# Kernel optimization log

Measured on AMD Instinct MI355X. Metric: run time of the kernel, lower is better.

## Reference

```python
import jax, jax.numpy as jnp
import numpy as np

EPS = 1e-5
PDIM, QKD, DIM = 64, 16, 256
SCALE = QKD ** -0.5


def setup_inputs() -> dict:
    key = jax.random.key(0)
    ks = jax.random.split(key, 13)
    B, H, W = 8, 64, 64
    return {
        "x": jax.random.normal(ks[0], (B, DIM, H, W), jnp.float32),
        "gn_g": jax.random.uniform(ks[1], (PDIM,), jnp.float32, 0.5, 1.5),
        "gn_b": jax.random.normal(ks[2], (PDIM,), jnp.float32) * 0.1,
        "qkv_w": jax.random.normal(ks[3], (2 * QKD + PDIM, PDIM), jnp.float32) * (PDIM ** -0.5),
        "qkv_bn_g": jax.random.uniform(ks[4], (2 * QKD + PDIM,), jnp.float32, 0.5, 1.5),
        "qkv_bn_b": jax.random.normal(ks[5], (2 * QKD + PDIM,), jnp.float32) * 0.1,
        "qkv_rm": jax.random.normal(ks[6], (2 * QKD + PDIM,), jnp.float32) * 0.1,
        "qkv_rv": jax.random.uniform(ks[7], (2 * QKD + PDIM,), jnp.float32, 0.5, 1.5),
        "proj_w": jax.random.normal(ks[8], (DIM, DIM), jnp.float32) * (DIM ** -0.5),
        "proj_bn_g": jax.random.uniform(ks[9], (DIM,), jnp.float32, 0.5, 1.5),
        "proj_bn_b": jax.random.normal(ks[10], (DIM,), jnp.float32) * 0.1,
        "proj_rm": jax.random.normal(ks[11], (DIM,), jnp.float32) * 0.1,
        "proj_rv": jax.random.uniform(ks[12], (DIM,), jnp.float32, 0.5, 1.5),
    }


def _bn(y, g, b, rm, rv):
    # inference BatchNorm over channel axis 1 of [B,C,H,W]
    inv = g / jnp.sqrt(rv + EPS)
    return y * inv[None, :, None, None] + (b - rm * inv)[None, :, None, None]


def reference(x, gn_g, gn_b, qkv_w, qkv_bn_g, qkv_bn_b, qkv_rm, qkv_rv,
              proj_w, proj_bn_g, proj_bn_b, proj_rm, proj_rv):
    B, C, H, W = x.shape
    x1, x2 = x[:, :PDIM], x[:, PDIM:]
    # GroupNorm with 1 group: normalize over (C,H,W) per sample
    mu = jnp.mean(x1, axis=(1, 2, 3), keepdims=True)
    var = jnp.var(x1, axis=(1, 2, 3), keepdims=True)
    x1n = (x1 - mu) / jnp.sqrt(var + EPS)
    x1n = x1n * gn_g[None, :, None, None] + gn_b[None, :, None, None]
    # qkv: 1x1 conv + BN
    qkv = jnp.einsum('bchw,oc->bohw', x1n, qkv_w)
    qkv = _bn(qkv, qkv_bn_g, qkv_bn_b, qkv_rm, qkv_rv)
    q, k, v = qkv[:, :QKD], qkv[:, QKD:2 * QKD], qkv[:, 2 * QKD:]
    N = H * W
    q = q.reshape(B, QKD, N)
    k = k.reshape(B, QKD, N)
    v = v.reshape(B, PDIM, N)
    attn = jnp.einsum('bcn,bcm->bnm', q, k) * SCALE  # [B,N,N]
    attn = jax.nn.softmax(attn, axis=-1)
    x1_attn = jnp.einsum('bcm,bnm->bcn', v, attn).reshape(B, PDIM, H, W)
    xc = jnp.concatenate([x1_attn, x2], axis=1)
    # proj: ReLU -> 1x1 conv -> BN
    y = jnp.einsum('bchw,oc->bohw', jax.nn.relu(xc), proj_w)
    return _bn(y, proj_bn_g, proj_bn_b, proj_rm, proj_rv)
```

## Files before the change

### kernel.cpp

```cpp
#include <hip/hip_runtime.h>
#include <hip/hip_bf16.h>

typedef __bf16 bf16;
typedef __bf16 bf16x4 __attribute__((ext_vector_type(4)));
typedef __bf16 bf16x8 __attribute__((ext_vector_type(8)));
typedef float  f32x16 __attribute__((ext_vector_type(16)));

#define MFMA32 __builtin_amdgcn_mfma_f32_32x32x16_bf16
#define EPSV 1e-5f
#define QSCALE 0.36067376022224085f

__device__ __forceinline__ f32x16 fzero16() {
  f32x16 z;
#pragma unroll
  for (int i = 0; i < 16; ++i) z[i] = 0.f;
  return z;
}

__device__ __forceinline__ void dma16(const void* g, void* s) {
  __builtin_amdgcn_global_load_lds(
      (const __attribute__((address_space(1))) void*)g,
      (__attribute__((address_space(3))) void*)s, 16, 0, 0);
}

__global__ __launch_bounds__(256) void k_stats_partial(const float* __restrict__ x,
                                                       float* __restrict__ part) {
  const int b = blockIdx.x >> 5, k = blockIdx.x & 31;
  const float* p = x + (size_t)b * 256 * 4096 + k * 8192;
  const int t = threadIdx.x;
  float s = 0.f, q = 0.f;
#pragma unroll
  for (int j = 0; j < 8; ++j) {
    float4 v = ((const float4*)p)[t + j * 256];
    s += v.x + v.y + v.z + v.w;
    q += v.x * v.x + v.y * v.y + v.z * v.z + v.w * v.w;
  }
  __shared__ float ls[256], lq[256];
  ls[t] = s; lq[t] = q;
  __syncthreads();
  for (int off = 128; off > 0; off >>= 1) {
    if (t < off) { ls[t] += ls[t + off]; lq[t] += lq[t + off]; }
    __syncthreads();
  }
  if (t == 0) { part[blockIdx.x * 2] = ls[0]; part[blockIdx.x * 2 + 1] = lq[0]; }
}

__global__ __launch_bounds__(256) void k_stats_final(const float* __restrict__ part,
                                                     float* __restrict__ stats) {
  const int t = threadIdx.x, b = t >> 5, k = t & 31;
  float s = part[(b * 32 + k) * 2], q = part[(b * 32 + k) * 2 + 1];
  for (int off = 16; off > 0; off >>= 1) {
    s += __shfl_down(s, off, 32);
    q += __shfl_down(q, off, 32);
  }
  if (k == 0) {
    const float inv_n = 1.f / 262144.f;
    const float mu = s * inv_n;
    const float var = q * inv_n - mu * mu;
    stats[b * 2] = mu;
    stats[b * 2 + 1] = rsqrtf(var + EPSV);
  }
}

__global__ __launch_bounds__(256) void k_qkv(
    const float* __restrict__ x, const float* __restrict__ gn_g, const float* __restrict__ gn_b,
    const float* __restrict__ qkv_w, const float* __restrict__ bn_g, const float* __restrict__ bn_b,
    const float* __restrict__ bn_rm, const float* __restrict__ bn_rv,
    const float* __restrict__ stats,
    bf16* __restrict__ qw, bf16* __restrict__ kw, bf16* __restrict__ vw) {
  const int b = blockIdx.x >> 6, tile = blockIdx.x & 63;
  const int n0 = tile * 64, t = threadIdx.x;
  __shared__ float xn[64][68];
  __shared__ float W[64][96];
  __shared__ float beta_s[96];
  const float mu = stats[b * 2], rstd = stats[b * 2 + 1];
  {
    const int c = t >> 2, f = t & 3;
    const float A = rstd * gn_g[c], B = gn_b[c] - mu * A;
    const float* xr = x + ((size_t)b * 256 + c) * 4096 + n0;
#pragma unroll
    for (int j = 0; j < 4; ++j) {
      float4 v = ((const float4*)xr)[f * 4 + j];
      const int nb = f * 16 + j * 4;
      xn[c][nb + 0] = v.x * A + B; xn[c][nb + 1] = v.y * A + B;
      xn[c][nb + 2] = v.z * A + B; xn[c][nb + 3] = v.w * A + B;
    }
  }
  for (int oc = t; oc < 96 * 8; oc += 256) {
    const int o = oc >> 3, ch = (oc & 7) * 8;
    const float inv = bn_g[o] * rsqrtf(bn_rv[o] + EPSV);
    if (ch == 0) beta_s[o] = bn_b[o] - bn_rm[o] * inv;
    const float* wr = qkv_w + o * 64 + ch;
#pragma unroll
    for (int i = 0; i < 8; ++i) W[ch + i][o] = wr[i] * inv;
  }
  __syncthreads();
  const int o_l = t & 31, ng = t >> 5;
#pragma unroll 1
  for (int p = 0; p < 3; ++p) {
    const int o = p * 32 + o_l;
    float acc[8];
#pragma unroll
    for (int j = 0; j < 8; ++j) acc[j] = 0.f;
    for (int c = 0; c < 64; ++c) {
      const float wv = W[c][o];
      const float* xr = &xn[c][ng * 8];
#pragma unroll
      for (int j = 0; j < 8; ++j) acc[j] += wv * xr[j];
    }
    const float beta = beta_s[o];
    const int nb = n0 + ng * 8;
    if (p == 0) {
      if (o < 16) {
#pragma unroll
        for (int j = 0; j < 8; ++j)
          qw[((size_t)b * 4096 + nb + j) * 16 + o] = (bf16)((acc[j] + beta) * QSCALE);
      } else {
#pragma unroll
        for (int j = 0; j < 8; ++j)
          kw[((size_t)b * 4096 + nb + j) * 16 + (o - 16)] = (bf16)(acc[j] + beta);
      }
    } else {
      const int c = (p - 1) * 32 + o_l;
      const int IT = nb >> 5;
      const int m4 = nb & 31;
      const int f  = ((m4 >> 4) << 1) + (c >> 5);
      const int b3 = (m4 >> 3) & 1;
      char* base = (char*)vw + (size_t)b * 524288 + (size_t)IT * 4096 +
                   f * 1024 + (c & 31) * 16 + b3 * 8;
      bf16x4 pk0, pk1;
#pragma unroll
      for (int i = 0; i < 4; ++i) {
        pk0[i] = (bf16)(acc[i] + beta);
        pk1[i] = (bf16)(acc[4 + i] + beta);
      }
      *(bf16x4*)base = pk0;
      *(bf16x4*)(base + 512) = pk1;
    }
  }
}

__global__ __launch_bounds__(256, 2) void k_attn(
    const bf16* __restrict__ qw, const bf16* __restrict__ kw,
    const bf16* __restrict__ vw, const float* __restrict__ x,
    bf16* __restrict__ xc) {
  __shared__ __align__(16) char smem[61440];
  const int orig = blockIdx.x;
  const int wg = (orig & 7) * 64 + (orig >> 3);
  const int b = wg >> 6, qblk = wg & 63;
  const int t = threadIdx.x;
  const int wid = t >> 6, l = t & 63, ln = l & 31, g = l >> 5;
  const int m0 = wid * 1024;

  const bf16* qb = qw + (size_t)b * 4096 * 16;
  const char* kb = (const char*)(kw + (size_t)b * 4096 * 16);
  const char* vfb = (const char*)vw + (size_t)b * 524288;

  const char* kdma = kb + (size_t)m0 * 32 + (2 * ln + g) * 16;
  const char* vdma = vfb + (size_t)(m0 >> 5) * 4096 + l * 16;
  char* ring = smem + wid * 15360;

  const int nq = qblk * 64 + ln;
  const bf16x8 qf0 = *(const bf16x8*)(qb + (size_t)nq * 16 + g * 8);
  const bf16x8 qf1 = *(const bf16x8*)(qb + (size_t)(nq + 32) * 16 + g * 8);
  asm volatile("" :: "v"(qf0), "v"(qf1));

  f32x16 O00 = fzero16(), O01 = fzero16();
  f32x16 O10 = fzero16(), O11 = fzero16();
  float l0 = 0.f, l1 = 0.f;

#define ISSUE_TILE(TI, SLOT)                                  \
  do {                                                        \
    char* dst = ring + (SLOT) * 5120;                         \
    const char* ks = kdma + (size_t)(TI) * 1024;              \
    const char* vs = vdma + (size_t)(TI) * 4096;              \
    dma16(ks, dst);                                           \
    dma16(vs, dst + 1024);                                    \
    dma16(vs + 1024, dst + 2048);                             \
    dma16(vs + 2048, dst + 3072);                             \
    dma16(vs + 3072, dst + 4096);                             \
  } while (0)

  ISSUE_TILE(0, 0);
  ISSUE_TILE(1, 1);
  ISSUE_TILE(2, 2);

  int slot = 0;
#pragma unroll 1
  for (int it = 0; it < 32; ++it) {
    const int rem = 31 - it;
    if (rem >= 2)      { asm volatile("s_waitcnt vmcnt(10)" ::: "memory"); }
    else if (rem == 1) { asm volatile("s_waitcnt vmcnt(5)"  ::: "memory"); }
    else               { asm volatile("s_waitcnt vmcnt(0)"  ::: "memory"); }
    const char* rb = ring + slot * 5120 + l * 16;
    const uint4 kc = *(const uint4*)rb;
    const uint4 v0 = *(const uint4*)(rb + 1024);
    const uint4 v1 = *(const uint4*)(rb + 2048);
    const uint4 v2 = *(const uint4*)(rb + 3072);
    const uint4 v3 = *(const uint4*)(rb + 4096);
    asm volatile("s_waitcnt lgkmcnt(0)" ::: "memory");
    if (it + 3 < 32) ISSUE_TILE(it + 3, slot);
    const bf16x8 kf = __builtin_bit_cast(bf16x8, kc);
    f32x16 S0 = MFMA32(kf, qf0, fzero16(), 0, 0, 0);
    f32x16 S1 = MFMA32(kf, qf1, fzero16(), 0, 0, 0);
#pragma unroll
    for (int r = 0; r < 16; ++r) S0[r] = __builtin_amdgcn_exp2f(S0[r]);
#pragma unroll
    for (int r = 0; r < 16; ++r) S1[r] = __builtin_amdgcn_exp2f(S1[r]);
    {
      float a[8], c[8];
#pragma unroll
      for (int r = 0; r < 8; ++r) { a[r] = S0[2 * r] + S0[2 * r + 1];
                                    c[r] = S1[2 * r] + S1[2 * r + 1]; }
#pragma unroll
      for (int r = 0; r < 4; ++r) { a[r] = a[2 * r] + a[2 * r + 1];
                                    c[r] = c[2 * r] + c[2 * r + 1]; }
      l0 += (a[0] + a[1]) + (a[2] + a[3]);
      l1 += (c[0] + c[1]) + (c[2] + c[3]);
    }
    bf16x8 pa0, pa1, pc0, pc1;
#pragma unroll
    for (int r = 0; r < 8; ++r) {
      pa0[r] = (bf16)S0[r]; pa1[r] = (bf16)S0[r + 8];
      pc0[r] = (bf16)S1[r]; pc1[r] = (bf16)S1[r + 8];
    }
    O00 = MFMA32(__builtin_bit_cast(bf16x8, v0), pa0, O00, 0, 0, 0);
    O10 = MFMA32(__builtin_bit_cast(bf16x8, v0), pc0, O10, 0, 0, 0);
    O01 = MFMA32(__builtin_bit_cast(bf16x8, v1), pa0, O01, 0, 0, 0);
    O11 = MFMA32(__builtin_bit_cast(bf16x8, v1), pc0, O11, 0, 0, 0);
    O00 = MFMA32(__builtin_bit_cast(bf16x8, v2), pa1, O00, 0, 0, 0);
    O10 = MFMA32(__builtin_bit_cast(bf16x8, v2), pc1, O10, 0, 0, 0);
    O01 = MFMA32(__builtin_bit_cast(bf16x8, v3), pa1, O01, 0, 0, 0);
    O11 = MFMA32(__builtin_bit_cast(bf16x8, v3), pc1, O11, 0, 0, 0);
    slot = (slot == 2) ? 0 : slot + 1;
  }
#undef ISSUE_TILE
  l0 += __shfl_xor(l0, 32, 64);
  l1 += __shfl_xor(l1, 32, 64);

  __syncthreads();

  {
    const int msk = 2 * (ln & 7);
#pragma unroll
    for (int hq = 0; hq < 2; ++hq) {
      char* orow = smem + (wid * 2 + hq) * 4096 + ln * 128;
#pragma unroll
      for (int hc = 0; hc < 2; ++hc) {
        const f32x16& O = hq ? (hc ? O11 : O10) : (hc ? O01 : O00);
#pragma unroll
        for (int j = 0; j < 4; ++j) {
          bf16x4 e;
#pragma unroll
          for (int i = 0; i < 4; ++i) e[i] = (bf16)O[4 * j + i];
          const int chunk = hc * 8 + 2 * j + g;
          *(bf16x4*)(orow + ((chunk ^ msk) << 3)) = e;
        }
      }
      if (g == 0) *(float*)(smem + 32768 + (wid * 2 + hq) * 128 + ln * 4) = hq ? l1 : l0;
    }
  }
  __syncthreads();

  {
    const int n = t >> 3, k8 = t & 7;
    const int off = ((2 * k8) ^ (2 * (n & 7))) << 3;
#pragma unroll
    for (int hq = 0; hq < 2; ++hq) {
      float L = 0.f;
      float acc[8];
#pragma unroll
      for (int e = 0; e < 8; ++e) acc[e] = 0.f;
#pragma unroll
      for (int kr_ = 0; kr_ < 4; ++kr_) {
        const int s = kr_ * 2 + hq;
        L += *(const float*)(smem + 32768 + s * 128 + n * 4);
        const bf16x8 v = *(const bf16x8*)(smem + s * 4096 + n * 128 + off);
#pragma unroll
        for (int e = 0; e < 8; ++e) acc[e] += (float)v[e];
      }
      const float rL = 1.0f / L;
      bf16x8 o8;
#pragma unroll
      for (int e = 0; e < 8; ++e) o8[e] = (bf16)fmaxf(acc[e] * rL, 0.f);
      *(bf16x8*)(xc + ((size_t)b * 4096 + qblk * 64 + hq * 32 + n) * 256 + k8 * 8) = o8;
    }
  }
  __syncthreads();

  {
    unsigned* tile_u = (unsigned*)smem;
    const float* xb = x + ((size_t)b * 256 + 64) * 4096 + qblk * 64;
#pragma unroll
    for (int i = 0; i < 6; ++i) {
      const int idx = i * 256 + t;
      const int cp = idx >> 4, f = idx & 15;
      const float4 a = *(const float4*)(xb + (size_t)(2 * cp) * 4096 + f * 4);
      const float4 c4 = *(const float4*)(xb + (size_t)(2 * cp + 1) * 4096 + f * 4);
      const float av[4] = {a.x, a.y, a.z, a.w};
      const float cv[4] = {c4.x, c4.y, c4.z, c4.w};
#pragma unroll
      for (int e = 0; e < 4; ++e) {
        const unsigned u =
            (unsigned)__builtin_bit_cast(unsigned short, (bf16)fmaxf(av[e], 0.f)) |
            ((unsigned)__builtin_bit_cast(unsigned short, (bf16)fmaxf(cv[e], 0.f)) << 16);
        tile_u[(f * 4 + e) * 97 + cp] = u;
      }
    }
    __syncthreads();
#pragma unroll
    for (int i = 0; i < 6; ++i) {
      const int idx = i * 256 + t;
      const int n = idx / 24, q = idx % 24;
      const uint4 d = *(const uint4*)&tile_u[n * 97 + q * 4];
      *(uint4*)(xc + ((size_t)b * 4096 + qblk * 64 + n) * 256 + 64 + q * 8) = d;
    }
  }
}

__global__ __launch_bounds__(256, 2) void k_proj(
    const bf16* __restrict__ xc, const float* __restrict__ pw,
    const float* __restrict__ bn_g, const float* __restrict__ bn_b,
    const float* __restrict__ bn_rm, const float* __restrict__ bn_rv,
    float* __restrict__ out) {
  const int orig = blockIdx.x;
  const int wg = (orig & 7) * 64 + (orig >> 3);
  const int b = wg >> 6, rem = wg & 63, nt = rem >> 1, oh = rem & 1;
  const int n0 = nt * 128, o0 = oh * 128;
  const int t = threadIdx.x, w = t >> 6, l = t & 63, ln = l & 31, g = l >> 5;

  __shared__ __align__(16) bf16 pws[128 * 256];
  __shared__ float beta_s[128];

  {
    const int o = t >> 1, half = t & 1;
    const float inv = bn_g[o0 + o] * rsqrtf(bn_rv[o0 + o] + EPSV);
    if (half == 0) beta_s[o] = bn_b[o0 + o] - bn_rm[o0 + o] * inv;
    const float* wr = pw + (size_t)(o0 + o) * 256 + half * 128;
    const int s_hh = (o & 15) * 8;
#pragma unroll
    for (int j = 0; j < 16; ++j) {
      const float4 a = ((const float4*)wr)[j * 2];
      const float4 c4 = ((const float4*)wr)[j * 2 + 1];
      bf16x8 v8;
      v8[0] = (bf16)(a.x * inv);  v8[1] = (bf16)(a.y * inv);
      v8[2] = (bf16)(a.z * inv);  v8[3] = (bf16)(a.w * inv);
      v8[4] = (bf16)(c4.x * inv); v8[5] = (bf16)(c4.y * inv);
      v8[6] = (bf16)(c4.z * inv); v8[7] = (bf16)(c4.w * inv);
      *(bf16x8*)&pws[o * 256 + ((half * 128 + j * 8) ^ s_hh)] = v8;
    }
  }
  __syncthreads();

  const bf16* xrow = xc + ((size_t)b * 4096 + n0 + w * 32 + ln) * 256;
  const int sw = (ln & 15) * 8;
  f32x16 acc0 = fzero16(), acc1 = fzero16(), acc2 = fzero16(), acc3 = fzero16();
#pragma unroll 4
  for (int ck = 0; ck < 256; ck += 16) {
    const bf16x8 bfrag = *(const bf16x8*)(xrow + ck + g * 8);
    const int cidx = (ck + g * 8) ^ sw;
    const bf16x8 a0 = *(const bf16x8*)&pws[(ln) * 256 + cidx];
    const bf16x8 a1 = *(const bf16x8*)&pws[(32 + ln) * 256 + cidx];
    const bf16x8 a2 = *(const bf16x8*)&pws[(64 + ln) * 256 + cidx];
    const bf16x8 a3 = *(const bf16x8*)&pws[(96 + ln) * 256 + cidx];
    acc0 = MFMA32(a0, bfrag, acc0, 0, 0, 0);
    acc1 = MFMA32(a1, bfrag, acc1, 0, 0, 0);
    acc2 = MFMA32(a2, bfrag, acc2, 0, 0, 0);
    acc3 = MFMA32(a3, bfrag, acc3, 0, 0, 0);
  }
  const int ncol = n0 + w * 32 + ln;
  float* ob = out + (size_t)b * 256 * 4096 + ncol;
#pragma unroll
  for (int og = 0; og < 4; ++og) {
    const f32x16& A = og == 0 ? acc0 : og == 1 ? acc1 : og == 2 ? acc2 : acc3;
#pragma unroll
    for (int r = 0; r < 16; ++r) {
      const int o_loc = og * 32 + (r & 3) + 8 * (r >> 2) + 4 * g;
      ob[(size_t)(o0 + o_loc) * 4096] = A[r] + beta_s[o_loc];
    }
  }
}

extern "C" void kernel_launch(void* const* d_in, const int* in_sizes, int n_in,
                              void* d_out, int out_size, void* d_ws, size_t ws_size,
                              hipStream_t stream) {
  (void)in_sizes; (void)n_in; (void)out_size; (void)ws_size;
  const float* x        = (const float*)d_in[0];
  const float* gn_g     = (const float*)d_in[1];
  const float* gn_b     = (const float*)d_in[2];
  const float* qkv_w    = (const float*)d_in[3];
  const float* qkv_bn_g = (const float*)d_in[4];
  const float* qkv_bn_b = (const float*)d_in[5];
  const float* qkv_rm   = (const float*)d_in[6];
  const float* qkv_rv   = (const float*)d_in[7];
  const float* proj_w   = (const float*)d_in[8];
  const float* proj_bn_g = (const float*)d_in[9];
  const float* proj_bn_b = (const float*)d_in[10];
  const float* proj_rm  = (const float*)d_in[11];
  const float* proj_rv  = (const float*)d_in[12];

  char* ws = (char*)d_ws;
  float* part  = (float*)ws;
  float* stats = (float*)(ws + 4096);
  bf16* qw = (bf16*)(ws + 8192);
  bf16* kw = (bf16*)(ws + 8192 + (1u << 20));
  bf16* vw = (bf16*)(ws + 8192 + (2u << 20));
  bf16* xc = (bf16*)(ws + 8192 + (6u << 20));

  k_stats_partial<<<256, 256, 0, stream>>>(x, part);
  k_stats_final<<<1, 256, 0, stream>>>(part, stats);
  k_qkv<<<512, 256, 0, stream>>>(x, gn_g, gn_b, qkv_w, qkv_bn_g, qkv_bn_b,
                                 qkv_rm, qkv_rv, stats, qw, kw, vw);
  k_attn<<<512, 256, 0, stream>>>(qw, kw, vw, x, xc);
  k_proj<<<512, 256, 0, stream>>>(xc, proj_w, proj_bn_g, proj_bn_b,
                                  proj_rm, proj_rv, (float*)d_out);
}
```

Before: 85.97 us.

## Fuse projection GEMM into attention kernel and precompute BN-folded proj weights

```diff
diff --git a/kernel.cpp b/kernel.cpp
--- a/kernel.cpp
+++ b/kernel.cpp
@@ -23,8 +23,24 @@
       (__attribute__((address_space(3))) void*)s, 16, 0, 0);
 }
 
-__global__ __launch_bounds__(256) void k_stats_partial(const float* __restrict__ x,
-                                                       float* __restrict__ part) {
+__global__ __launch_bounds__(256) void k_stats_partial(
+    const float* __restrict__ x, const float* __restrict__ pw,
+    const float* __restrict__ pg, const float* __restrict__ prv,
+    const float* __restrict__ prm, const float* __restrict__ pbb,
+    float* __restrict__ part, bf16* __restrict__ pwb, float* __restrict__ pwbeta) {
+  if (blockIdx.x >= 256) {
+    const int pb = blockIdx.x - 256;
+    const int t = threadIdx.x;
+    const int o = pb * 4 + (t >> 6), cseg = (t & 63) * 4;
+    const float inv = pg[o] * rsqrtf(prv[o] + EPSV);
+    const float4 v = *(const float4*)(pw + (size_t)o * 256 + cseg);
+    bf16x4 pk;
+    pk[0] = (bf16)(v.x * inv); pk[1] = (bf16)(v.y * inv);
+    pk[2] = (bf16)(v.z * inv); pk[3] = (bf16)(v.w * inv);
+    *(bf16x4*)(pwb + (size_t)o * 256 + cseg) = pk;
+    if ((t & 63) == 0) pwbeta[o] = pbb[o] - prm[o] * inv;
+    return;
+  }
   const int b = blockIdx.x >> 5, k = blockIdx.x & 31;
   const float* p = x + (size_t)b * 256 * 4096 + k * 8192;
   const int t = threadIdx.x;
@@ -140,11 +156,12 @@
   }
 }
 
-__global__ __launch_bounds__(256, 2) void k_attn(
+__global__ __launch_bounds__(256, 2) void k_attn_fused(
     const bf16* __restrict__ qw, const bf16* __restrict__ kw,
     const bf16* __restrict__ vw, const float* __restrict__ x,
-    bf16* __restrict__ xc) {
-  __shared__ __align__(16) char smem[61440];
+    const bf16* __restrict__ pwb, const float* __restrict__ pwbeta,
+    float* __restrict__ out) {
+  __shared__ __align__(16) char smem[70656];
   const int orig = blockIdx.x;
   const int wg = (orig & 7) * 64 + (orig >> 3);
   const int b = wg >> 6, qblk = wg & 63;
@@ -260,36 +277,9 @@
       if (g == 0) *(float*)(smem + 32768 + (wid * 2 + hq) * 128 + ln * 4) = hq ? l1 : l0;
     }
   }
-  __syncthreads();
 
   {
-    const int n = t >> 3, k8 = t & 7;
-    const int off = ((2 * k8) ^ (2 * (n & 7))) << 3;
-#pragma unroll
-    for (int hq = 0; hq < 2; ++hq) {
-      float L = 0.f;
-      float acc[8];
-#pragma unroll
-      for (int e = 0; e < 8; ++e) acc[e] = 0.f;
-#pragma unroll
-      for (int kr_ = 0; kr_ < 4; ++kr_) {
-        const int s = kr_ * 2 + hq;
-        L += *(const float*)(smem + 32768 + s * 128 + n * 4);
-        const bf16x8 v = *(const bf16x8*)(smem + s * 4096 + n * 128 + off);
-#pragma unroll
-        for (int e = 0; e < 8; ++e) acc[e] += (float)v[e];
-      }
-      const float rL = 1.0f / L;
-      bf16x8 o8;
-#pragma unroll
-      for (int e = 0; e < 8; ++e) o8[e] = (bf16)fmaxf(acc[e] * rL, 0.f);
-      *(bf16x8*)(xc + ((size_t)b * 4096 + qblk * 64 + hq * 32 + n) * 256 + k8 * 8) = o8;
-    }
-  }
-  __syncthreads();
-
-  {
-    unsigned* tile_u = (unsigned*)smem;
+    unsigned* xcw = (unsigned*)(smem + 36864);
     const float* xb = x + ((size_t)b * 256 + 64) * 4096 + qblk * 64;
 #pragma unroll
     for (int i = 0; i < 6; ++i) {
@@ -301,82 +291,82 @@
       const float cv[4] = {c4.x, c4.y, c4.z, c4.w};
 #pragma unroll
       for (int e = 0; e < 4; ++e) {
+        const int n = f * 4 + e;
         const unsigned u =
             (unsigned)__builtin_bit_cast(unsigned short, (bf16)fmaxf(av[e], 0.f)) |
             ((unsigned)__builtin_bit_cast(unsigned short, (bf16)fmaxf(cv[e], 0.f)) << 16);
-        tile_u[(f * 4 + e) * 97 + cp] = u;
-      }
-    }
-    __syncthreads();
-#pragma unroll
-    for (int i = 0; i < 6; ++i) {
-      const int idx = i * 256 + t;
-      const int n = idx / 24, q = idx % 24;
-      const uint4 d = *(const uint4*)&tile_u[n * 97 + q * 4];
-      *(uint4*)(xc + ((size_t)b * 4096 + qblk * 64 + n) * 256 + 64 + q * 8) = d;
-    }
-  }
-}
-
-__global__ __launch_bounds__(256, 2) void k_proj(
-    const bf16* __restrict__ xc, const float* __restrict__ pw,
-    const float* __restrict__ bn_g, const float* __restrict__ bn_b,
-    const float* __restrict__ bn_rm, const float* __restrict__ bn_rv,
-    float* __restrict__ out) {
-  const int orig = blockIdx.x;
-  const int wg = (orig & 7) * 64 + (orig >> 3);
-  const int b = wg >> 6, rem = wg & 63, nt = rem >> 1, oh = rem & 1;
-  const int n0 = nt * 128, o0 = oh * 128;
-  const int t = threadIdx.x, w = t >> 6, l = t & 63, ln = l & 31, g = l >> 5;
-
-  __shared__ __align__(16) bf16 pws[128 * 256];
-  __shared__ float beta_s[128];
+        xcw[n * 128 + ((32 + cp) ^ ((n & 15) * 4))] = u;
+      }
+    }
+  }
+  __syncthreads();
 
   {
-    const int o = t >> 1, half = t & 1;
-    const float inv = bn_g[o0 + o] * rsqrtf(bn_rv[o0 + o] + EPSV);
-    if (half == 0) beta_s[o] = bn_b[o0 + o] - bn_rm[o0 + o] * inv;
-    const float* wr = pw + (size_t)(o0 + o) * 256 + half * 128;
-    const int s_hh = (o & 15) * 8;
-#pragma unroll
-    for (int j = 0; j < 16; ++j) {
-      const float4 a = ((const float4*)wr)[j * 2];
-      const float4 c4 = ((const float4*)wr)[j * 2 + 1];
-      bf16x8 v8;
-      v8[0] = (bf16)(a.x * inv);  v8[1] = (bf16)(a.y * inv);
-      v8[2] = (bf16)(a.z * inv);  v8[3] = (bf16)(a.w * inv);
-      v8[4] = (bf16)(c4.x * inv); v8[5] = (bf16)(c4.y * inv);
-      v8[6] = (bf16)(c4.z * inv); v8[7] = (bf16)(c4.w * inv);
-      *(bf16x8*)&pws[o * 256 + ((half * 128 + j * 8) ^ s_hh)] = v8;
-    }
+    const int n = t >> 3, k8 = t & 7;
+    const int off = ((2 * k8) ^ (2 * (n & 7))) << 3;
+    char* xcb = smem + 36864;
+#pragma unroll
+    for (int hq = 0; hq < 2; ++hq) {
+      float L = 0.f;
+      float acc[8];
+#pragma unroll
+      for (int e = 0; e < 8; ++e) acc[e] = 0.f;
+#pragma unroll
+      for (int kr_ = 0; kr_ < 4; ++kr_) {
+        const int s = kr_ * 2 + hq;
+        L += *(const float*)(smem + 32768 + s * 128 + n * 4);
+        const bf16x8 v = *(const bf16x8*)(smem + s * 4096 + n * 128 + off);
+#pragma unroll
+        for (int e = 0; e < 8; ++e) acc[e] += (float)v[e];
+      }
+      const float rL = 1.0f / L;
+      bf16x8 o8;
+#pragma unroll
+      for (int e = 0; e < 8; ++e) o8[e] = (bf16)fmaxf(acc[e] * rL, 0.f);
+      const int n2 = hq * 32 + n;
+      *(bf16x8*)(xcb + n2 * 512 + ((k8 ^ (n & 15)) * 16)) = o8;
+    }
+    ((float*)(smem + 69632))[t] = pwbeta[t];
   }
   __syncthreads();
 
-  const bf16* xrow = xc + ((size_t)b * 4096 + n0 + w * 32 + ln) * 256;
-  const int sw = (ln & 15) * 8;
-  f32x16 acc0 = fzero16(), acc1 = fzero16(), acc2 = fzero16(), acc3 = fzero16();
-#pragma unroll 4
-  for (int ck = 0; ck < 256; ck += 16) {
-    const bf16x8 bfrag = *(const bf16x8*)(xrow + ck + g * 8);
-    const int cidx = (ck + g * 8) ^ sw;
-    const bf16x8 a0 = *(const bf16x8*)&pws[(ln) * 256 + cidx];
-    const bf16x8 a1 = *(const bf16x8*)&pws[(32 + ln) * 256 + cidx];
-    const bf16x8 a2 = *(const bf16x8*)&pws[(64 + ln) * 256 + cidx];
-    const bf16x8 a3 = *(const bf16x8*)&pws[(96 + ln) * 256 + cidx];
-    acc0 = MFMA32(a0, bfrag, acc0, 0, 0, 0);
-    acc1 = MFMA32(a1, bfrag, acc1, 0, 0, 0);
-    acc2 = MFMA32(a2, bfrag, acc2, 0, 0, 0);
-    acc3 = MFMA32(a3, bfrag, acc3, 0, 0, 0);
-  }
-  const int ncol = n0 + w * 32 + ln;
-  float* ob = out + (size_t)b * 256 * 4096 + ncol;
-#pragma unroll
-  for (int og = 0; og < 4; ++og) {
-    const f32x16& A = og == 0 ? acc0 : og == 1 ? acc1 : og == 2 ? acc2 : acc3;
-#pragma unroll
-    for (int r = 0; r < 16; ++r) {
-      const int o_loc = og * 32 + (r & 3) + 8 * (r >> 2) + 4 * g;
-      ob[(size_t)(o0 + o_loc) * 4096] = A[r] + beta_s[o_loc];
+  {
+    bf16* pwlds = (bf16*)smem;
+    const char* xcb = smem + 36864;
+    const float* beta_l = (const float*)(smem + 69632);
+    const int osub = wid >> 1, nsub = wid & 1;
+    const int n2 = nsub * 32 + ln;
+    float* ob = out + (size_t)b * 256 * 4096 + qblk * 64 + n2;
+#pragma unroll 1
+    for (int ch = 0; ch < 4; ++ch) {
+      {
+        const int o = t >> 2, q4 = t & 3;
+        const bf16* src = pwb + (size_t)(ch * 64 + o) * 256 + q4 * 64;
+        const int sw = (o & 15) * 8;
+#pragma unroll
+        for (int j = 0; j < 8; ++j) {
+          const bf16x8 v = *(const bf16x8*)(src + j * 8);
+          *(bf16x8*)&pwlds[o * 256 + ((q4 * 64 + j * 8) ^ sw)] = v;
+        }
+      }
+      __syncthreads();
+      f32x16 acc = fzero16();
+      const int o = osub * 32 + ln;
+      const int swo = (o & 15) * 8;
+#pragma unroll
+      for (int ks = 0; ks < 16; ++ks) {
+        const bf16x8 af = *(const bf16x8*)&pwlds[o * 256 + ((ks * 16 + g * 8) ^ swo)];
+        const bf16x8 bf_ = *(const bf16x8*)(xcb + n2 * 512 +
+                                            (((2 * ks + g) ^ (n2 & 15)) * 16));
+        acc = MFMA32(af, bf_, acc, 0, 0, 0);
+      }
+#pragma unroll
+      for (int r = 0; r < 16; ++r) {
+        const int o_loc = (r & 3) + 8 * (r >> 2) + 4 * g;
+        const int og = ch * 64 + osub * 32 + o_loc;
+        ob[(size_t)og * 4096] = acc[r] + beta_l[og];
+      }
+      if (ch < 3) __syncthreads();
     }
   }
 }
@@ -400,18 +390,19 @@
   const float* proj_rv  = (const float*)d_in[12];
 
   char* ws = (char*)d_ws;
-  float* part  = (float*)ws;
-  float* stats = (float*)(ws + 4096);
-  bf16* qw = (bf16*)(ws + 8192);
-  bf16* kw = (bf16*)(ws + 8192 + (1u << 20));
-  bf16* vw = (bf16*)(ws + 8192 + (2u << 20));
-  bf16* xc = (bf16*)(ws + 8192 + (6u << 20));
-
-  k_stats_partial<<<256, 256, 0, stream>>>(x, part);
+  float* part   = (float*)ws;
+  float* stats  = (float*)(ws + 4096);
+  bf16* qw      = (bf16*)(ws + 8192);
+  bf16* kw      = (bf16*)(ws + 8192 + (1u << 20));
+  bf16* vw      = (bf16*)(ws + 8192 + (2u << 20));
+  bf16* pwb     = (bf16*)(ws + 8192 + (6u << 20));
+  float* pwbeta = (float*)(ws + 8192 + (6u << 20) + 131072);
+
+  k_stats_partial<<<320, 256, 0, stream>>>(x, proj_w, proj_bn_g, proj_rv,
+                                           proj_rm, proj_bn_b, part, pwb, pwbeta);
   k_stats_final<<<1, 256, 0, stream>>>(part, stats);
   k_qkv<<<512, 256, 0, stream>>>(x, gn_g, gn_b, qkv_w, qkv_bn_g, qkv_bn_b,
                                  qkv_rm, qkv_rv, stats, qw, kw, vw);
-  k_attn<<<512, 256, 0, stream>>>(qw, kw, vw, x, xc);
-  k_proj<<<512, 256, 0, stream>>>(xc, proj_w, proj_bn_g, proj_bn_b,
-                                  proj_rm, proj_rv, (float*)d_out);
-}
+  k_attn_fused<<<512, 256, 0, stream>>>(qw, kw, vw, x, pwb, pwbeta,
+                                        (float*)d_out);
+}
```

Measured after the change: 81.06 us. 5.7% less time.
